# Kernel tuning notes

Measured on AMD Instinct MI355X. Metric: run time of the kernel, lower is better.

## Reference

```python
import jax, jax.numpy as jnp
import numpy as np

B, NV, NS, L = 32, 2048, 512, 64
FEAT, SEM, HID, ATT, DM = 1024, 512, 512, 512, 512


def setup_inputs() -> dict:
    key = jax.random.key(0)
    ks = jax.random.split(key, 14)
    s = lambda k, sh: jax.random.normal(k, sh, dtype=jnp.float32) * 0.02
    return {
        "query": jax.random.normal(ks[0], (B, 1, HID), dtype=jnp.float32),
        "visual_features": jax.random.normal(ks[1], (B, NV, FEAT), dtype=jnp.float32),
        "semantic_features": jax.random.normal(ks[2], (B, NS, SEM), dtype=jnp.float32),
        "patient_info": jax.random.normal(ks[3], (B, L, DM), dtype=jnp.float32),
        "W1v": s(ks[4], (HID, ATT)),
        "W2v": s(ks[5], (FEAT, ATT)),
        "vv": s(ks[6], (ATT, 1)),
        "W3": s(ks[7], (DM, ATT)),
        "b3": jnp.zeros((ATT,), dtype=jnp.float32),
        "W1s": s(ks[8], (HID, ATT)),
        "W2s": s(ks[9], (SEM, ATT)),
        "vs": s(ks[10], (ATT, 1)),
        "W": s(ks[11], (FEAT + SEM, FEAT)),
        "bW": jnp.zeros((FEAT,), dtype=jnp.float32),
    }


def reference(query, visual_features, semantic_features, patient_info,
              W1v, W2v, vv, W3, b3, W1s, W2s, vs, W, bW):
    # mean over patient sequence, project: [B,1,ATT]
    pinfo = jnp.mean(patient_info, axis=1, keepdims=True) @ W3 + b3
    q_v = query @ W1v          # [B,1,ATT]
    # visual branch
    v_scores = jnp.tanh(q_v + visual_features @ W2v + pinfo) @ vv  # [B,NV,1]
    v_attn = jax.nn.softmax(v_scores, axis=1)
    # semantic branch
    q_s = query @ W1s
    s_scores = jnp.tanh(q_s + semantic_features @ W2s + pinfo) @ vs  # [B,NS,1]
    s_attn = jax.nn.softmax(s_scores, axis=1)
    ctx = jnp.concatenate([
        jnp.sum(visual_features * v_attn, axis=1),    # [B,FEAT]
        jnp.sum(semantic_features * s_attn, axis=1),  # [B,SEM]
    ], axis=1) @ W + bW
    return ctx, v_attn, s_attn
```

## Files before the change

### kernel.cpp

```cpp
#include <hip/hip_runtime.h>

typedef float f32x4 __attribute__((ext_vector_type(4)));
typedef short short8 __attribute__((ext_vector_type(8)));

#define B_    32
#define NV_   2048
#define NS_   512
#define L_    64
#define FEAT_ 1024
#define SEM_  512
#define HID_  512
#define ATT_  512
#define DM_   512

__device__ __forceinline__ unsigned int f2bf_pk(float lo, float hi) {
  unsigned int ul = (__float_as_uint(lo) + 0x8000u) >> 16;
  unsigned int uh = (__float_as_uint(hi) + 0x8000u) & 0xffff0000u;
  return uh | ul;
}

__device__ __forceinline__ unsigned short f2bf(float f) {
  return (unsigned short)((__float_as_uint(f) + 0x8000u) >> 16);
}

__device__ __forceinline__ float bflo(unsigned int u) { return __uint_as_float(u << 16); }
__device__ __forceinline__ float bfhi(unsigned int u) { return __uint_as_float(u & 0xffff0000u); }

__device__ __forceinline__ float fast_tanh(float x) {
  float e = __expf(2.f * x);
  return 1.f - 2.f * __builtin_amdgcn_rcpf(e + 1.f);
}

__device__ __forceinline__ void gll16(const void* g, void* l) {
  __builtin_amdgcn_global_load_lds(
      (const __attribute__((address_space(1))) unsigned int*)g,
      (__attribute__((address_space(3))) unsigned int*)l, 16, 0, 0);
}

__global__ __launch_bounds__(256) void k_pmean(const float* __restrict__ pat,
                                               float* __restrict__ pm) {
  int b = blockIdx.x, t = threadIdx.x;
  for (int d = t; d < DM_; d += 256) {
    float s = 0.f;
    for (int l = 0; l < L_; ++l) s += pat[(b * L_ + l) * DM_ + d];
    pm[b * DM_ + d] = s * (1.f / 64.f);
  }
}

__global__ __launch_bounds__(256) void k_qp(const float* __restrict__ query,
                                            const float* __restrict__ pm,
                                            const float* __restrict__ W1v,
                                            const float* __restrict__ W1s,
                                            const float* __restrict__ W3,
                                            const float* __restrict__ b3,
                                            float* __restrict__ qpv,
                                            float* __restrict__ qps) {
  int idx = blockIdx.x * 256 + threadIdx.x;
  int b = idx >> 9, a = idx & 511;
  float pi = b3[a];
  for (int d = 0; d < DM_; ++d) pi += pm[b * DM_ + d] * W3[d * ATT_ + a];
  float qv = 0.f, qs = 0.f;
  for (int h = 0; h < HID_; ++h) {
    float q = query[b * HID_ + h];
    qv += q * W1v[h * ATT_ + a];
    qs += q * W1s[h * ATT_ + a];
  }
  qpv[idx] = qv + pi;
  qps[idx] = qs + pi;
}

__global__ __launch_bounds__(256) void k_swz(const float* __restrict__ W2,
                                             unsigned short* __restrict__ out,
                                             int total) {
  int idx = blockIdx.x * 256 + threadIdx.x;
  if (idx >= total) return;
  int k = idx >> 9, c = idx & 511;
  int kc = k >> 5, kr = k & 31, q = kr >> 3, j = kr & 7;
  int cb = c >> 4, n = c & 15;
  out[(kc * 32 + cb) * 512 + q * 128 + n * 8 + j] = f2bf(W2[idx]);
}

__global__ __launch_bounds__(256) void k_cvtA(const float* __restrict__ X,
                                              unsigned short* __restrict__ out,
                                              int K) {
  const int rt = blockIdx.x, kc = blockIdx.y, nkc = K >> 5;
  const int t = threadIdx.x;
  uint4* dst = (uint4*)(out + ((size_t)rt * nkc + kc) * 4096);
#pragma unroll
  for (int p = 0; p < 2; ++p) {
    int c = p * 256 + t;
    int rb = c >> 6, q = (c >> 4) & 3, m = c & 15;
    int row = rt * 128 + rb * 16 + m;
    const float4* src = (const float4*)(X + (size_t)row * K + kc * 32 + q * 8);
    float4 v0 = src[0], v1 = src[1];
    uint4 o;
    o.x = f2bf_pk(v0.x, v0.y);
    o.y = f2bf_pk(v0.z, v0.w);
    o.z = f2bf_pk(v1.x, v1.y);
    o.w = f2bf_pk(v1.z, v1.w);
    dst[c] = o;
  }
}

__global__ __launch_bounds__(256) void k_scores_bf16(const unsigned short* __restrict__ Aswz,
                                                     const unsigned short* __restrict__ Wt,
                                                     const float* __restrict__ qp,
                                                     const float* __restrict__ vvec,
                                                     float* __restrict__ score,
                                                     int K, int rows_per_batch) {
  __shared__ __align__(16) unsigned short As[4096];
  __shared__ __align__(16) unsigned short Bs[4096];
  const int t = threadIdx.x;
  const int lane = t & 63;
  const int wave = t >> 6;
  const int wr = wave & 1, wc = wave >> 1;
  const int quad = lane >> 4, l15 = lane & 15;
  const int ct = blockIdx.x;
  const int rt = blockIdx.y;
  const int row0 = rt * 128;
  const int b = row0 / rows_per_batch;
  const int nk = K >> 5;

  char* ldsA = (char*)As + wave * 1024;
  char* ldsB = (char*)Bs + wave * 1024;
  const char* gA = (const char*)(Aswz + (size_t)rt * nk * 4096) + t * 16;
  const char* gB = (const char*)Wt + (size_t)ct * 8192 + t * 16;

  const f32x4 zero = {0.f, 0.f, 0.f, 0.f};
  f32x4 acc[4][4];
#pragma unroll
  for (int a = 0; a < 4; ++a)
#pragma unroll
    for (int bb = 0; bb < 4; ++bb) acc[a][bb] = zero;

  for (int kc = 0; kc < nk; ++kc) {
    __syncthreads();
    gll16(gA, ldsA);
    gll16(gA + 4096, ldsA + 4096);
    gll16(gB, ldsB);
    gll16(gB + 4096, ldsB + 4096);
    gA += 8192;
    gB += 32768;
    __syncthreads();
    short8 af[4], bfr[4];
#pragma unroll
    for (int a = 0; a < 4; ++a)
      af[a] = *(const short8*)(As + (wr * 4 + a) * 512 + quad * 128 + l15 * 8);
#pragma unroll
    for (int bb = 0; bb < 4; ++bb)
      bfr[bb] = *(const short8*)(Bs + (wc * 4 + bb) * 512 + quad * 128 + l15 * 8);
#pragma unroll
    for (int a = 0; a < 4; ++a)
#pragma unroll
      for (int bb = 0; bb < 4; ++bb)
        acc[a][bb] = __builtin_amdgcn_mfma_f32_16x16x32_bf16(af[a], bfr[bb], acc[a][bb], 0, 0, 0);
  }

  const int colbase = ct * 128 + wc * 64;
  float qv_[4], vw_[4];
#pragma unroll
  for (int bb = 0; bb < 4; ++bb) {
    int col = colbase + bb * 16 + l15;
    qv_[bb] = qp[b * ATT_ + col];
    vw_[bb] = vvec[col];
  }
#pragma unroll
  for (int a = 0; a < 4; ++a) {
#pragma unroll
    for (int r = 0; r < 4; ++r) {
      float s = 0.f;
#pragma unroll
      for (int bb = 0; bb < 4; ++bb)
        s += fast_tanh(acc[a][bb][r] + qv_[bb]) * vw_[bb];
      s += __shfl_xor(s, 1);
      s += __shfl_xor(s, 2);
      s += __shfl_xor(s, 4);
      s += __shfl_xor(s, 8);
      if (l15 == 0) {
        int row = row0 + wr * 64 + a * 16 + quad * 4 + r;
        atomicAdd(&score[row], s);
      }
    }
  }
}

__global__ __launch_bounds__(256) void k_scores_f32(const float* __restrict__ X,
                                                    const unsigned short* __restrict__ Wt,
                                                    const float* __restrict__ qp,
                                                    const float* __restrict__ vvec,
                                                    float* __restrict__ score,
                                                    int K, int rows_per_batch) {
  __shared__ __align__(16) unsigned short As[4096];
  __shared__ __align__(16) unsigned short Bs[4096];
  const int t = threadIdx.x;
  const int lane = t & 63;
  const int wave = t >> 6;
  const int wr = wave & 1, wc = wave >> 1;
  const int quad = lane >> 4, l15 = lane & 15;
  const int row0 = blockIdx.x * 128;
  const int ct = blockIdx.y;
  const int b = row0 / rows_per_batch;

  const int ai_row = t >> 3;
  const int ai_k0 = (t & 7) * 4;
  const int a_q = ai_k0 >> 3;
  const int a_j0 = ai_k0 & 7;

  const f32x4 zero = {0.f, 0.f, 0.f, 0.f};
  f32x4 acc[4][4];
#pragma unroll
  for (int a = 0; a < 4; ++a)
#pragma unroll
    for (int bb = 0; bb < 4; ++bb) acc[a][bb] = zero;

  const int nk = K >> 5;
  for (int kc = 0; kc < nk; ++kc) {
    __syncthreads();
#pragma unroll
    for (int ii = 0; ii < 4; ++ii) {
      int i = ii * 32 + ai_row;
      const float4 v = *(const float4*)(X + (size_t)(row0 + i) * K + kc * 32 + ai_k0);
      uint2 h;
      h.x = f2bf_pk(v.x, v.y);
      h.y = f2bf_pk(v.z, v.w);
      int rb = i >> 4, m = i & 15;
      *(uint2*)(As + rb * 512 + a_q * 128 + m * 8 + a_j0) = h;
    }
    {
      const uint4* src = (const uint4*)(Wt + (size_t)(kc * 32 + ct * 8) * 512);
      uint4* dst = (uint4*)Bs;
      dst[t] = src[t];
      dst[t + 256] = src[t + 256];
    }
    __syncthreads();
    short8 af[4], bfr[4];
#pragma unroll
    for (int a = 0; a < 4; ++a)
      af[a] = *(const short8*)(As + (wr * 4 + a) * 512 + quad * 128 + l15 * 8);
#pragma unroll
    for (int bb = 0; bb < 4; ++bb)
      bfr[bb] = *(const short8*)(Bs + (wc * 4 + bb) * 512 + quad * 128 + l15 * 8);
#pragma unroll
    for (int a = 0; a < 4; ++a)
#pragma unroll
      for (int bb = 0; bb < 4; ++bb)
        acc[a][bb] = __builtin_amdgcn_mfma_f32_16x16x32_bf16(af[a], bfr[bb], acc[a][bb], 0, 0, 0);
  }

  const int colbase = ct * 128 + wc * 64;
  float qv_[4], vw_[4];
#pragma unroll
  for (int bb = 0; bb < 4; ++bb) {
    int col = colbase + bb * 16 + l15;
    qv_[bb] = qp[b * ATT_ + col];
    vw_[bb] = vvec[col];
  }
#pragma unroll
  for (int a = 0; a < 4; ++a) {
#pragma unroll
    for (int r = 0; r < 4; ++r) {
      float s = 0.f;
#pragma unroll
      for (int bb = 0; bb < 4; ++bb)
        s += fast_tanh(acc[a][bb][r] + qv_[bb]) * vw_[bb];
      s += __shfl_xor(s, 1);
      s += __shfl_xor(s, 2);
      s += __shfl_xor(s, 4);
      s += __shfl_xor(s, 8);
      if (l15 == 0) {
        int row = row0 + wr * 64 + a * 16 + quad * 4 + r;
        atomicAdd(&score[row], s);
      }
    }
  }
}

__global__ __launch_bounds__(256) void k_softmax(const float* __restrict__ score,
                                                 float* __restrict__ attn, int N) {
  __shared__ float sm[4];
  int b = blockIdx.x, t = threadIdx.x;
  const float* s = score + (size_t)b * N;
  float m = -1e30f;
  for (int i = t; i < N; i += 256) m = fmaxf(m, s[i]);
  for (int k = 32; k; k >>= 1) m = fmaxf(m, __shfl_xor(m, k));
  if ((t & 63) == 0) sm[t >> 6] = m;
  __syncthreads();
  m = fmaxf(fmaxf(sm[0], sm[1]), fmaxf(sm[2], sm[3]));
  __syncthreads();
  float sum = 0.f;
  for (int i = t; i < N; i += 256) sum += __expf(s[i] - m);
  for (int k = 32; k; k >>= 1) sum += __shfl_xor(sum, k);
  if ((t & 63) == 0) sm[t >> 6] = sum;
  __syncthreads();
  sum = sm[0] + sm[1] + sm[2] + sm[3];
  float inv = 1.f / sum;
  for (int i = t; i < N; i += 256) attn[(size_t)b * N + i] = __expf(s[i] - m) * inv;
}

__global__ __launch_bounds__(256) void k_wsum_swz(const unsigned short* __restrict__ Aswz,
                                                  const float* __restrict__ attn,
                                                  float* __restrict__ ctx_pre,
                                                  int nkc, int rtPerBatch,
                                                  int rowsPerBatch, int colOff) {
  const int b = blockIdx.x, kc = blockIdx.y;
  const int t = threadIdx.x, q = t >> 6, l = t & 63;
  const int rbl = l >> 4, m = l & 15;
  float acc[8] = {0.f, 0.f, 0.f, 0.f, 0.f, 0.f, 0.f, 0.f};
  for (int rt = 0; rt < rtPerBatch; ++rt) {
    const unsigned short* blk = Aswz + ((size_t)(b * rtPerBatch + rt) * nkc + kc) * 4096;
    const float* ab = attn + (size_t)b * rowsPerBatch + rt * 128;
#pragma unroll
    for (int p = 0; p < 2; ++p) {
      int rb = p * 4 + rbl;
      float a = ab[rb * 16 + m];
      uint4 v = *(const uint4*)(blk + rb * 512 + q * 128 + m * 8);
      acc[0] += a * bflo(v.x);
      acc[1] += a * bfhi(v.x);
      acc[2] += a * bflo(v.y);
      acc[3] += a * bfhi(v.y);
      acc[4] += a * bflo(v.z);
      acc[5] += a * bfhi(v.z);
      acc[6] += a * bflo(v.w);
      acc[7] += a * bfhi(v.w);
    }
  }
#pragma unroll
  for (int off = 1; off < 64; off <<= 1) {
#pragma unroll
    for (int j = 0; j < 8; ++j) acc[j] += __shfl_xor(acc[j], off);
  }
  if (l == 0) {
    float* dst = ctx_pre + b * 1536 + colOff + kc * 32 + q * 8;
#pragma unroll
    for (int j = 0; j < 8; ++j) dst[j] = acc[j];
  }
}

__global__ __launch_bounds__(256) void k_wsum(const float* __restrict__ feats,
                                              const float* __restrict__ attn,
                                              float* __restrict__ ctx_pre,
                                              int N, int F, int colOff, int rowsPerChunk) {
  int b = blockIdx.x, rc = blockIdx.y, t = threadIdx.x;
  int c4 = t * 4;
  if (c4 >= F) return;
  int r0 = rc * rowsPerChunk;
  const float* fb = feats + ((size_t)b * N + r0) * F;
  const float* ab = attn + (size_t)b * N + r0;
  float4 acc = {0.f, 0.f, 0.f, 0.f};
  for (int r = 0; r < rowsPerChunk; ++r) {
    float a = ab[r];
    float4 v = *(const float4*)(fb + (size_t)r * F + c4);
    acc.x += a * v.x; acc.y += a * v.y; acc.z += a * v.z; acc.w += a * v.w;
  }
  float* dst = ctx_pre + b * 1536 + colOff + c4;
  atomicAdd(dst + 0, acc.x);
  atomicAdd(dst + 1, acc.y);
  atomicAdd(dst + 2, acc.z);
  atomicAdd(dst + 3, acc.w);
}

__global__ __launch_bounds__(256) void k_final(const float* __restrict__ cp,
                                               const float* __restrict__ W,
                                               const float* __restrict__ bW,
                                               float* __restrict__ out) {
  int b = blockIdx.x, oc = blockIdx.y, t = threadIdx.x;
  int o = oc * 256 + t;
  float acc = bW[o];
  const float* c = cp + b * 1536;
  for (int k = 0; k < 1536; ++k) acc += c[k] * W[k * FEAT_ + o];
  out[b * FEAT_ + o] = acc;
}

extern "C" void kernel_launch(void* const* d_in, const int* in_sizes, int n_in,
                              void* d_out, int out_size, void* d_ws, size_t ws_size,
                              hipStream_t stream) {
  const float* query = (const float*)d_in[0];
  const float* vf    = (const float*)d_in[1];
  const float* sf    = (const float*)d_in[2];
  const float* pat   = (const float*)d_in[3];
  const float* W1v   = (const float*)d_in[4];
  const float* W2v   = (const float*)d_in[5];
  const float* vv    = (const float*)d_in[6];
  const float* W3    = (const float*)d_in[7];
  const float* b3    = (const float*)d_in[8];
  const float* W1s   = (const float*)d_in[9];
  const float* W2s   = (const float*)d_in[10];
  const float* vs    = (const float*)d_in[11];
  const float* W     = (const float*)d_in[12];
  const float* bW    = (const float*)d_in[13];
  float* out = (float*)d_out;

  char* ws = (char*)d_ws;
  float* scores_v = (float*)(ws);
  float* scores_s = (float*)(ws + 262144);
  float* ctx_pre  = (float*)(ws + 327680);
  float* pm   = (float*)(ws + 524288);
  float* qpv  = (float*)(ws + 589824);
  float* qps  = (float*)(ws + 655360);
  unsigned short* Wtv = (unsigned short*)(ws + 720896);
  unsigned short* Wts = (unsigned short*)(ws + 720896 + 1048576);
  unsigned short* Av  = (unsigned short*)(ws + 4194304);
  unsigned short* Asm = (unsigned short*)(ws + 4194304 + 134217728);
  const size_t NEED = 4194304ull + 134217728ull + 16777216ull;
  const bool bf16path = (ws_size >= NEED);

  hipMemsetAsync(d_ws, 0, bf16path ? 327680 : 524288, stream);

  k_pmean<<<32, 256, 0, stream>>>(pat, pm);
  k_qp<<<64, 256, 0, stream>>>(query, pm, W1v, W1s, W3, b3, qpv, qps);
  k_swz<<<(FEAT_ * ATT_) / 256, 256, 0, stream>>>(W2v, Wtv, FEAT_ * ATT_);
  k_swz<<<(SEM_ * ATT_) / 256, 256, 0, stream>>>(W2s, Wts, SEM_ * ATT_);

  float* v_attn = out + B_ * FEAT_;
  float* s_attn = out + B_ * FEAT_ + B_ * NV_;

  if (bf16path) {
    k_cvtA<<<dim3((B_ * NV_) / 128, FEAT_ / 32), 256, 0, stream>>>(vf, Av, FEAT_);
    k_cvtA<<<dim3((B_ * NS_) / 128, SEM_ / 32), 256, 0, stream>>>(sf, Asm, SEM_);
    k_scores_bf16<<<dim3(4, (B_ * NV_) / 128), 256, 0, stream>>>(Av, Wtv, qpv, vv, scores_v, FEAT_, NV_);
    k_scores_bf16<<<dim3(4, (B_ * NS_) / 128), 256, 0, stream>>>(Asm, Wts, qps, vs, scores_s, SEM_, NS_);
    k_softmax<<<B_, 256, 0, stream>>>(scores_v, v_attn, NV_);
    k_softmax<<<B_, 256, 0, stream>>>(scores_s, s_attn, NS_);
    k_wsum_swz<<<dim3(B_, FEAT_ / 32), 256, 0, stream>>>(Av, v_attn, ctx_pre, FEAT_ / 32, NV_ / 128, NV_, 0);
    k_wsum_swz<<<dim3(B_, SEM_ / 32), 256, 0, stream>>>(Asm, s_attn, ctx_pre, SEM_ / 32, NS_ / 128, NS_, 1024);
  } else {
    k_scores_f32<<<dim3((B_ * NV_) / 128, 4), 256, 0, stream>>>(vf, Wtv, qpv, vv, scores_v, FEAT_, NV_);
    k_scores_f32<<<dim3((B_ * NS_) / 128, 4), 256, 0, stream>>>(sf, Wts, qps, vs, scores_s, SEM_, NS_);
    k_softmax<<<B_, 256, 0, stream>>>(scores_v, v_attn, NV_);
    k_softmax<<<B_, 256, 0, stream>>>(scores_s, s_attn, NS_);
    k_wsum<<<dim3(B_, 8), 256, 0, stream>>>(vf, v_attn, ctx_pre, NV_, FEAT_, 0, 256);
    k_wsum<<<dim3(B_, 2), 256, 0, stream>>>(sf, s_attn, ctx_pre, NS_, SEM_, 1024, 256);
  }

  k_final<<<dim3(B_, 4), 256, 0, stream>>>(ctx_pre, W, bW, out);
}
```

Measured before the change: 778.1 us.

## Fuse fp32-to-bf16 conversion into the scores GEMM and widen column tiles

Replaces the separate conversion kernel plus bf16 scores GEMM with one fused kernel. It reads fp32 activations directly, converts them to bf16 in registers, stages them in LDS and also writes the swizzled bf16 copy that the later weighted-sum kernel needs. Each block now covers 64 rows and all 512 columns, so the activations are read once instead of once per column tile. B fragments are loaded straight from global memory into registers instead of through LDS. This removes a full write and re-read of the bf16 activation buffer and one launch, at the cost of more accumulator registers (4x8 tiles) and global-latency-bound B loads with no double buffering.

New measurement: 685.8 us. 11.9% less time.

```diff
diff --git a/kernel.cpp b/kernel.cpp
--- a/kernel.cpp
+++ b/kernel.cpp
@@ -29,12 +29,6 @@
 __device__ __forceinline__ float fast_tanh(float x) {
   float e = __expf(2.f * x);
   return 1.f - 2.f * __builtin_amdgcn_rcpf(e + 1.f);
-}
-
-__device__ __forceinline__ void gll16(const void* g, void* l) {
-  __builtin_amdgcn_global_load_lds(
-      (const __attribute__((address_space(1))) unsigned int*)g,
-      (__attribute__((address_space(3))) unsigned int*)l, 16, 0, 0);
 }
 
 __global__ __launch_bounds__(256) void k_pmean(const float* __restrict__ pat,
@@ -80,106 +74,87 @@
   out[(kc * 32 + cb) * 512 + q * 128 + n * 8 + j] = f2bf(W2[idx]);
 }
 
-__global__ __launch_bounds__(256) void k_cvtA(const float* __restrict__ X,
-                                              unsigned short* __restrict__ out,
-                                              int K) {
-  const int rt = blockIdx.x, kc = blockIdx.y, nkc = K >> 5;
+__global__ __launch_bounds__(256, 2) void k_scores_fused(
+    const float* __restrict__ X, const unsigned short* __restrict__ Wt,
+    const float* __restrict__ qp, const float* __restrict__ vvec,
+    float* __restrict__ score, unsigned short* __restrict__ Av,
+    int K, int rows_per_batch) {
+  __shared__ __align__(16) unsigned short As[2048];
   const int t = threadIdx.x;
-  uint4* dst = (uint4*)(out + ((size_t)rt * nkc + kc) * 4096);
-#pragma unroll
-  for (int p = 0; p < 2; ++p) {
-    int c = p * 256 + t;
-    int rb = c >> 6, q = (c >> 4) & 3, m = c & 15;
-    int row = rt * 128 + rb * 16 + m;
-    const float4* src = (const float4*)(X + (size_t)row * K + kc * 32 + q * 8);
-    float4 v0 = src[0], v1 = src[1];
+  const int lane = t & 63, wave = t >> 6;
+  const int quad = lane >> 4, l15 = lane & 15;
+  const int row0 = blockIdx.x * 64;
+  const int b = row0 / rows_per_batch;
+  const int nk = K >> 5;
+  const int rt128 = blockIdx.x >> 1;
+  const int rbOff = (blockIdx.x & 1) * 4;
+
+  const int r = t >> 2, q_ = t & 3;
+  const int arb = r >> 4, am = r & 15;
+  const float* gA = X + (size_t)(row0 + r) * K + q_ * 8;
+  uint4* asDst = (uint4*)(As + arb * 512 + q_ * 128 + am * 8);
+  char* avBase = (char*)(Av + (size_t)rt128 * nk * 4096) +
+                 (rbOff + arb) * 1024 + q_ * 256 + am * 16;
+
+  const char* gB = (const char*)Wt + (size_t)wave * 8192 + lane * 16;
+
+  const f32x4 zero = {0.f, 0.f, 0.f, 0.f};
+  f32x4 acc[4][8];
+#pragma unroll
+  for (int a = 0; a < 4; ++a)
+#pragma unroll
+    for (int cb = 0; cb < 8; ++cb) acc[a][cb] = zero;
+
+  for (int kc = 0; kc < nk; ++kc) {
+    short8 bfr[8];
+    const char* gBk = gB + (size_t)kc * 32768;
+#pragma unroll
+    for (int cb = 0; cb < 8; ++cb)
+      bfr[cb] = *(const short8*)(gBk + cb * 1024);
+
+    __syncthreads();
+    const float4 v0 = *(const float4*)(gA + kc * 32);
+    const float4 v1 = *(const float4*)(gA + kc * 32 + 4);
     uint4 o;
     o.x = f2bf_pk(v0.x, v0.y);
     o.y = f2bf_pk(v0.z, v0.w);
     o.z = f2bf_pk(v1.x, v1.y);
     o.w = f2bf_pk(v1.z, v1.w);
-    dst[c] = o;
-  }
-}
-
-__global__ __launch_bounds__(256) void k_scores_bf16(const unsigned short* __restrict__ Aswz,
-                                                     const unsigned short* __restrict__ Wt,
-                                                     const float* __restrict__ qp,
-                                                     const float* __restrict__ vvec,
-                                                     float* __restrict__ score,
-                                                     int K, int rows_per_batch) {
-  __shared__ __align__(16) unsigned short As[4096];
-  __shared__ __align__(16) unsigned short Bs[4096];
-  const int t = threadIdx.x;
-  const int lane = t & 63;
-  const int wave = t >> 6;
-  const int wr = wave & 1, wc = wave >> 1;
-  const int quad = lane >> 4, l15 = lane & 15;
-  const int ct = blockIdx.x;
-  const int rt = blockIdx.y;
-  const int row0 = rt * 128;
-  const int b = row0 / rows_per_batch;
-  const int nk = K >> 5;
-
-  char* ldsA = (char*)As + wave * 1024;
-  char* ldsB = (char*)Bs + wave * 1024;
-  const char* gA = (const char*)(Aswz + (size_t)rt * nk * 4096) + t * 16;
-  const char* gB = (const char*)Wt + (size_t)ct * 8192 + t * 16;
-
-  const f32x4 zero = {0.f, 0.f, 0.f, 0.f};
-  f32x4 acc[4][4];
-#pragma unroll
-  for (int a = 0; a < 4; ++a)
-#pragma unroll
-    for (int bb = 0; bb < 4; ++bb) acc[a][bb] = zero;
-
-  for (int kc = 0; kc < nk; ++kc) {
+    *asDst = o;
+    *(uint4*)(avBase + (size_t)kc * 8192) = o;
     __syncthreads();
-    gll16(gA, ldsA);
-    gll16(gA + 4096, ldsA + 4096);
-    gll16(gB, ldsB);
-    gll16(gB + 4096, ldsB + 4096);
-    gA += 8192;
-    gB += 32768;
-    __syncthreads();
-    short8 af[4], bfr[4];
+
+    short8 af[4];
 #pragma unroll
     for (int a = 0; a < 4; ++a)
-      af[a] = *(const short8*)(As + (wr * 4 + a) * 512 + quad * 128 + l15 * 8);
-#pragma unroll
-    for (int bb = 0; bb < 4; ++bb)
-      bfr[bb] = *(const short8*)(Bs + (wc * 4 + bb) * 512 + quad * 128 + l15 * 8);
+      af[a] = *(const short8*)(As + a * 512 + quad * 128 + l15 * 8);
 #pragma unroll
     for (int a = 0; a < 4; ++a)
 #pragma unroll
-      for (int bb = 0; bb < 4; ++bb)
-        acc[a][bb] = __builtin_amdgcn_mfma_f32_16x16x32_bf16(af[a], bfr[bb], acc[a][bb], 0, 0, 0);
-  }
-
-  const int colbase = ct * 128 + wc * 64;
-  float qv_[4], vw_[4];
-#pragma unroll
-  for (int bb = 0; bb < 4; ++bb) {
-    int col = colbase + bb * 16 + l15;
-    qv_[bb] = qp[b * ATT_ + col];
-    vw_[bb] = vvec[col];
+      for (int cb = 0; cb < 8; ++cb)
+        acc[a][cb] = __builtin_amdgcn_mfma_f32_16x16x32_bf16(af[a], bfr[cb], acc[a][cb], 0, 0, 0);
+  }
+
+  float qv_[8], vw_[8];
+#pragma unroll
+  for (int cb = 0; cb < 8; ++cb) {
+    int col = wave * 128 + cb * 16 + l15;
+    qv_[cb] = qp[b * ATT_ + col];
+    vw_[cb] = vvec[col];
   }
 #pragma unroll
   for (int a = 0; a < 4; ++a) {
 #pragma unroll
-    for (int r = 0; r < 4; ++r) {
+    for (int rr = 0; rr < 4; ++rr) {
       float s = 0.f;
 #pragma unroll
-      for (int bb = 0; bb < 4; ++bb)
-        s += fast_tanh(acc[a][bb][r] + qv_[bb]) * vw_[bb];
+      for (int cb = 0; cb < 8; ++cb)
+        s += fast_tanh(acc[a][cb][rr] + qv_[cb]) * vw_[cb];
       s += __shfl_xor(s, 1);
       s += __shfl_xor(s, 2);
       s += __shfl_xor(s, 4);
       s += __shfl_xor(s, 8);
-      if (l15 == 0) {
-        int row = row0 + wr * 64 + a * 16 + quad * 4 + r;
-        atomicAdd(&score[row], s);
-      }
+      if (l15 == 0) atomicAdd(&score[row0 + a * 16 + quad * 4 + rr], s);
     }
   }
 }
@@ -415,10 +390,8 @@
   float* s_attn = out + B_ * FEAT_ + B_ * NV_;
 
   if (bf16path) {
-    k_cvtA<<<dim3((B_ * NV_) / 128, FEAT_ / 32), 256, 0, stream>>>(vf, Av, FEAT_);
-    k_cvtA<<<dim3((B_ * NS_) / 128, SEM_ / 32), 256, 0, stream>>>(sf, Asm, SEM_);
-    k_scores_bf16<<<dim3(4, (B_ * NV_) / 128), 256, 0, stream>>>(Av, Wtv, qpv, vv, scores_v, FEAT_, NV_);
-    k_scores_bf16<<<dim3(4, (B_ * NS_) / 128), 256, 0, stream>>>(Asm, Wts, qps, vs, scores_s, SEM_, NS_);
+    k_scores_fused<<<(B_ * NV_) / 64, 256, 0, stream>>>(vf, Wtv, qpv, vv, scores_v, Av, FEAT_, NV_);
+    k_scores_fused<<<(B_ * NS_) / 64, 256, 0, stream>>>(sf, Wts, qps, vs, scores_s, Asm, SEM_, NS_);
     k_softmax<<<B_, 256, 0, stream>>>(scores_v, v_attn, NV_);
     k_softmax<<<B_, 256, 0, stream>>>(scores_s, s_attn, NS_);
     k_wsum_swz<<<dim3(B_, FEAT_ / 32), 256, 0, stream>>>(Av, v_attn, ctx_pre, FEAT_ / 32, NV_ / 128, NV_, 0);
```
